# Optimization experiments

Measured on AMD Instinct MI355X. Metric: run time of the kernel, lower is better.

Reference implementation:

```python
import jax, jax.numpy as jnp
import numpy as np

N = 4096
K = 8


def setup_inputs() -> dict:
    key = jax.random.key(0)
    kA, kb, ka, kZ, kC = jax.random.split(key, 5)
    A = (jax.random.uniform(kA, (N, N)) < 0.01).astype(jnp.float32)
    beta = jax.random.normal(kb, (N,), dtype=jnp.float32)
    a = jax.random.normal(ka, (1,), dtype=jnp.float32)
    Z = jax.random.normal(kZ, (K, N), dtype=jnp.float32)
    C = jax.random.normal(kC, (N, K), dtype=jnp.float32)
    return {"A": A, "beta": beta, "a": a, "Z": Z, "C": C}


def reference(A, beta, a, Z, C):
    # beta_ij = beta_i + beta_j  -> [N, N]
    beta2 = beta[:, None] + beta[None, :]
    Zs = jax.nn.softmax(Z, axis=0)          # [K, N], softmax over archetypes
    Cs = jax.nn.softmax(C, axis=0)          # [N, K], softmax over nodes
    # M = (Zs @ Cs @ Zs).T -> [N, K] latent positions
    M = (Zs @ (Cs @ Zs)).T
    # Pairwise euclidean distance with the original's +1e-6 shift inside the square.
    diff = M[:, None, :] - M[None, :, :] + 1e-6   # [N, N, K]
    z_dist = jnp.sqrt(jnp.sum(diff * diff, axis=-1))  # [N, N]
    theta = beta2 - a[0] * z_dist
    sp = jax.nn.softplus(theta)
    # Zero the diagonal (theta - diag(diagonal(theta)) zeroes diag entries).
    d = jnp.arange(N)
    theta_off = theta.at[d, d].set(0.0)
    sp_off = sp.at[d, d].set(0.0)
    LL = jnp.sum(theta_off * A) - jnp.sum(sp_off)
    return LL
```

## Files before the change

### kernel.cpp

```cpp
#include <hip/hip_runtime.h>

#define N 4096
#define K 8
#define RB 64
#define CB 256
#define RCH 16
#define NCH (RB / RCH)
#define NPB 16

__device__ __forceinline__ float fast_exp2(float x) { return __builtin_amdgcn_exp2f(x); }
__device__ __forceinline__ float fast_log2(float x) { return __builtin_amdgcn_logf(x); }
__device__ __forceinline__ float fast_sqrt(float x) { return __builtin_amdgcn_sqrtf(x); }

__device__ __forceinline__ void load_lds_16B(const float* g, float* l) {
    __builtin_amdgcn_global_load_lds((const __attribute__((address_space(1))) void*)g,
                                     (__attribute__((address_space(3))) void*)l,
                                     16, 0, 0);
}

__global__ __launch_bounds__(256) void prep_stats(
    const float* __restrict__ Z, const float* __restrict__ C,
    const float* __restrict__ A, const float* __restrict__ beta,
    const float* __restrict__ a_ptr,
    float* __restrict__ ZsT, float* __restrict__ Upart, float* __restrict__ out)
{
    const int t = threadIdx.x;
    const int n = blockIdx.x * 256 + t;
    const float L2E = 1.44269504f;
    const float LN2 = 0.69314718f;

    __shared__ float zsL[256 * K];
    __shared__ float eL[256 * K];
    __shared__ float red[4][64];
    __shared__ float dsum[4];

    const float av_diag = A[(size_t)n * N + n];
    const float bn = beta[n];
    const float a_v = a_ptr[0];

    float z[K];
#pragma unroll
    for (int k = 0; k < K; ++k) z[k] = Z[k * N + n];
    float zmax = z[0];
#pragma unroll
    for (int k = 1; k < K; ++k) zmax = fmaxf(zmax, z[k]);
    float zs[K];
    float zsum = 0.f;
#pragma unroll
    for (int k = 0; k < K; ++k) { zs[k] = fast_exp2((z[k] - zmax) * L2E); zsum += zs[k]; }
    const float inv = 1.f / zsum;
#pragma unroll
    for (int k = 0; k < K; ++k) zs[k] *= inv;

    float4* zst_p = (float4*)(ZsT + (size_t)n * K);
    zst_p[0] = make_float4(zs[0], zs[1], zs[2], zs[3]);
    zst_p[1] = make_float4(zs[4], zs[5], zs[6], zs[7]);

    const float4* c_p = (const float4*)(C + (size_t)n * K);
    const float4 c0 = c_p[0], c1 = c_p[1];
    float e[K];
    e[0] = fast_exp2(c0.x * L2E); e[1] = fast_exp2(c0.y * L2E);
    e[2] = fast_exp2(c0.z * L2E); e[3] = fast_exp2(c0.w * L2E);
    e[4] = fast_exp2(c1.x * L2E); e[5] = fast_exp2(c1.y * L2E);
    e[6] = fast_exp2(c1.z * L2E); e[7] = fast_exp2(c1.w * L2E);

#pragma unroll
    for (int k = 0; k < K; ++k) { zsL[t * K + k] = zs[k]; eL[t * K + k] = e[k]; }
    __syncthreads();

    const int cell = t & 63, q = t >> 6;
    const int a = cell >> 3, b = cell & 7;
    float s = 0.f;
    const int n0 = q * 64;
#pragma unroll 4
    for (int nn = 0; nn < 64; ++nn)
        s = fmaf(zsL[(n0 + nn) * K + a], eL[(n0 + nn) * K + b], s);
    red[q][cell] = s;
    __syncthreads();
    if (t < 64)
        Upart[blockIdx.x * 64 + t] = red[0][t] + red[1][t] + red[2][t] + red[3][t];

    const float theta = fmaf(-a_v, 2.8284271247e-6f, 2.f * bn);
    const float ex = fast_exp2(theta * L2E);
    const float sp = LN2 * fast_log2(1.f + ex);
    float d = fmaf(theta, av_diag, -sp);
    for (int off = 32; off > 0; off >>= 1) d += __shfl_down(d, off, 64);
    const int lane = t & 63, wd = t >> 6;
    if (lane == 0) dsum[wd] = d;
    __syncthreads();
    if (t == 0) atomicAdd(out, -(dsum[0] + dsum[1] + dsum[2] + dsum[3]));
}

__global__ __launch_bounds__(256) void pair_ll(
    const float* __restrict__ A, const float* __restrict__ beta,
    const float* __restrict__ a_ptr, const float* __restrict__ ZsT,
    const float* __restrict__ Upart, float* __restrict__ out)
{
    const int t = threadIdx.x;
    const int lane = t & 63, w = t >> 6;
    const int i0 = blockIdx.x * RB;
    const int jbase = blockIdx.y * CB;
    const int j = jbase + t;
    const float L2E = 1.44269504f;
    const float LN2 = 0.69314718f;

    __shared__ __align__(16) float Abuf[2][RCH][CB];
    __shared__ __align__(16) float4 ntwoMi[RB][2];
    __shared__ __align__(8)  float2 rc[RB];
    __shared__ float UL[64];
    __shared__ float wsum[4];

    {
        const float* g = A + (size_t)(i0 + w * 4) * N + jbase + lane * 4;
#pragma unroll
        for (int rr = 0; rr < 4; ++rr)
            load_lds_16B(g + (size_t)rr * N, &Abuf[0][w * 4 + rr][0]);
    }

    if (t < 64) {
        float s = 0.f;
#pragma unroll
        for (int blk = 0; blk < NPB; ++blk) s += Upart[blk * 64 + t];
        UL[t] = s;
    }
    __syncthreads();

    float sinv[8];
#pragma unroll
    for (int b = 0; b < 8; ++b) {
        float s = 0.f;
#pragma unroll
        for (int a = 0; a < 8; ++a) s += UL[a * 8 + b];
        sinv[b] = 1.f / s;
    }

    const float4* zp = (const float4*)(ZsT + (size_t)j * K);
    const float4 z0 = zp[0], z1 = zp[1];
    float wv[K] = { z0.x * sinv[0], z0.y * sinv[1], z0.z * sinv[2], z0.w * sinv[3],
                    z1.x * sinv[4], z1.y * sinv[5], z1.z * sinv[6], z1.w * sinv[7] };
    float mj[K];
#pragma unroll
    for (int k = 0; k < K; ++k) {
        float acc = 0.f;
#pragma unroll
        for (int kk = 0; kk < K; ++kk) acc = fmaf(UL[k * K + kk], wv[kk], acc);
        mj[k] = acc;
    }
    float mj2 = mj[0] * mj[0];
#pragma unroll
    for (int k = 1; k < K; ++k) mj2 = fmaf(mj[k], mj[k], mj2);
    const float bjL2E = beta[j] * L2E;
    const float naL2E = -a_ptr[0] * L2E;

    if (t < RB) {
        const float4* zp2 = (const float4*)(ZsT + (size_t)(i0 + t) * K);
        const float4 y0 = zp2[0], y1 = zp2[1];
        float wr[K] = { y0.x * sinv[0], y0.y * sinv[1], y0.z * sinv[2], y0.w * sinv[3],
                        y1.x * sinv[4], y1.y * sinv[5], y1.z * sinv[6], y1.w * sinv[7] };
        float v[K];
#pragma unroll
        for (int k = 0; k < K; ++k) {
            float acc = 0.f;
#pragma unroll
            for (int kk = 0; kk < K; ++kk) acc = fmaf(UL[k * K + kk], wr[kk], acc);
            v[k] = acc + 1e-6f;
        }
        float s2 = 0.f;
#pragma unroll
        for (int k = 0; k < K; ++k) s2 = fmaf(v[k], v[k], s2);
        ntwoMi[t][0] = make_float4(-2.f * v[0], -2.f * v[1], -2.f * v[2], -2.f * v[3]);
        ntwoMi[t][1] = make_float4(-2.f * v[4], -2.f * v[5], -2.f * v[6], -2.f * v[7]);
        rc[t] = make_float2(s2, beta[i0 + t] * L2E);
    }
    __syncthreads();

    float acc_t = 0.f, acc_l = 0.f;
    int buf = 0;
    for (int c = 0; c < NCH; ++c) {
        if (c + 1 < NCH) {
            const float* g = A + (size_t)(i0 + (c + 1) * RCH + w * 4) * N + jbase + lane * 4;
#pragma unroll
            for (int rr = 0; rr < 4; ++rr)
                load_lds_16B(g + (size_t)rr * N, &Abuf[buf ^ 1][w * 4 + rr][0]);
        }
#pragma unroll
        for (int r = 0; r < RCH; ++r) {
            const int ir = c * RCH + r;
            const float av = Abuf[buf][r][t];
            const float4 tm0 = ntwoMi[ir][0];
            const float4 tm1 = ntwoMi[ir][1];
            const float2 cc = rc[ir];
            float ss = cc.x + mj2;
            ss = fmaf(tm0.x, mj[0], ss); ss = fmaf(tm0.y, mj[1], ss);
            ss = fmaf(tm0.z, mj[2], ss); ss = fmaf(tm0.w, mj[3], ss);
            ss = fmaf(tm1.x, mj[4], ss); ss = fmaf(tm1.y, mj[5], ss);
            ss = fmaf(tm1.z, mj[6], ss); ss = fmaf(tm1.w, mj[7], ss);
            ss = fmaxf(ss, 0.f);
            const float dist = fast_sqrt(ss);
            const float t2 = fmaf(naL2E, dist, cc.y + bjL2E);
            const float ex = fast_exp2(t2);
            const float lp = fast_log2(1.f + ex);
            acc_t = fmaf(t2, av, acc_t);
            acc_l += lp;
        }
        if (c + 1 < NCH) __syncthreads();
        buf ^= 1;
    }
    float acc = LN2 * (acc_t - acc_l);

    for (int off = 32; off > 0; off >>= 1) acc += __shfl_down(acc, off, 64);
    if (lane == 0) wsum[w] = acc;
    __syncthreads();
    if (t == 0) atomicAdd(out, wsum[0] + wsum[1] + wsum[2] + wsum[3]);
}

extern "C" void kernel_launch(void* const* d_in, const int* in_sizes, int n_in,
                              void* d_out, int out_size, void* d_ws, size_t ws_size,
                              hipStream_t stream)
{
    const float* A    = (const float*)d_in[0];
    const float* beta = (const float*)d_in[1];
    const float* a    = (const float*)d_in[2];
    const float* Z    = (const float*)d_in[3];
    const float* C    = (const float*)d_in[4];
    float* out = (float*)d_out;

    float* ws    = (float*)d_ws;
    float* ZsT   = ws;
    float* Upart = ws + (size_t)N * K;

    hipMemsetAsync(out, 0, sizeof(float), stream);
    prep_stats<<<NPB, 256, 0, stream>>>(Z, C, A, beta, a, ZsT, Upart, out);

    dim3 grid(N / RB, N / CB);
    pair_ll<<<grid, 256, 0, stream>>>(A, beta, a, ZsT, Upart, out);
}
```

Baseline: 115.7 us.

## Exploit pair symmetry: compute only upper-triangular tiles with transposed A

Result: slower. 121.5 us (+5.1%).

```diff
diff --git a/kernel.cpp b/kernel.cpp
--- a/kernel.cpp
+++ b/kernel.cpp
@@ -2,10 +2,11 @@
 
 #define N 4096
 #define K 8
-#define RB 64
-#define CB 256
+#define TB 128
+#define NT (N / TB)
 #define RCH 16
-#define NCH (RB / RCH)
+#define NCH (TB / RCH)
+#define TP 129
 #define NPB 16
 
 __device__ __forceinline__ float fast_exp2(float x) { return __builtin_amdgcn_exp2f(x); }
@@ -20,23 +21,15 @@
 
 __global__ __launch_bounds__(256) void prep_stats(
     const float* __restrict__ Z, const float* __restrict__ C,
-    const float* __restrict__ A, const float* __restrict__ beta,
-    const float* __restrict__ a_ptr,
-    float* __restrict__ ZsT, float* __restrict__ Upart, float* __restrict__ out)
+    float* __restrict__ ZsT, float* __restrict__ Upart)
 {
     const int t = threadIdx.x;
     const int n = blockIdx.x * 256 + t;
     const float L2E = 1.44269504f;
-    const float LN2 = 0.69314718f;
 
     __shared__ float zsL[256 * K];
     __shared__ float eL[256 * K];
     __shared__ float red[4][64];
-    __shared__ float dsum[4];
-
-    const float av_diag = A[(size_t)n * N + n];
-    const float bn = beta[n];
-    const float a_v = a_ptr[0];
 
     float z[K];
 #pragma unroll
@@ -79,16 +72,6 @@
     __syncthreads();
     if (t < 64)
         Upart[blockIdx.x * 64 + t] = red[0][t] + red[1][t] + red[2][t] + red[3][t];
-
-    const float theta = fmaf(-a_v, 2.8284271247e-6f, 2.f * bn);
-    const float ex = fast_exp2(theta * L2E);
-    const float sp = LN2 * fast_log2(1.f + ex);
-    float d = fmaf(theta, av_diag, -sp);
-    for (int off = 32; off > 0; off >>= 1) d += __shfl_down(d, off, 64);
-    const int lane = t & 63, wd = t >> 6;
-    if (lane == 0) dsum[wd] = d;
-    __syncthreads();
-    if (t == 0) atomicAdd(out, -(dsum[0] + dsum[1] + dsum[2] + dsum[3]));
 }
 
 __global__ __launch_bounds__(256) void pair_ll(
@@ -96,26 +79,85 @@
     const float* __restrict__ a_ptr, const float* __restrict__ ZsT,
     const float* __restrict__ Upart, float* __restrict__ out)
 {
+    const int ti = blockIdx.x, tj = blockIdx.y;
+    if (ti > tj) return;
+    const bool dTile = (ti == tj);
+
     const int t = threadIdx.x;
     const int lane = t & 63, w = t >> 6;
-    const int i0 = blockIdx.x * RB;
-    const int jbase = blockIdx.y * CB;
-    const int j = jbase + t;
+    const int i0 = ti * TB, jb = tj * TB;
+    const int jl = t & 127, h = t >> 7;
+    const int j = jb + jl;
     const float L2E = 1.44269504f;
     const float LN2 = 0.69314718f;
 
-    __shared__ __align__(16) float Abuf[2][RCH][CB];
-    __shared__ __align__(16) float4 ntwoMi[RB][2];
-    __shared__ __align__(8)  float2 rc[RB];
+    __shared__ __align__(16) float Abuf[2][RCH][TB];
+    __shared__ float Tbuf[2][RCH][TP];
+    __shared__ __align__(16) float4 ntwoMi[TB][2];
+    __shared__ __align__(8)  float2 rc[TB];
     __shared__ float UL[64];
     __shared__ float wsum[4];
 
-    {
-        const float* g = A + (size_t)(i0 + w * 4) * N + jbase + lane * 4;
-#pragma unroll
-        for (int rr = 0; rr < 4; ++rr)
-            load_lds_16B(g + (size_t)rr * N, &Abuf[0][w * 4 + rr][0]);
-    }
+#define STAGE_ABUF(B, CH)                                                          \
+    {                                                                              \
+        const float* g_ = A + (size_t)(i0 + (CH) * RCH + w * 4 + (lane >> 5)) * N  \
+                          + jb + (lane & 31) * 4;                                  \
+        load_lds_16B(g_,         &Abuf[B][w * 4][0]);                              \
+        load_lds_16B(g_ + 2 * N, &Abuf[B][w * 4 + 2][0]);                          \
+    }
+
+#define STAGE_TREG(CH)                                                             \
+    {                                                                              \
+        const float* g_ = A + (size_t)(jb + (t >> 1)) * N + i0 + (CH) * RCH        \
+                          + (t & 1) * 8;                                           \
+        tr0 = *(const float4*)(g_);                                                \
+        tr1 = *(const float4*)(g_ + 4);                                            \
+    }
+
+#define TBUF_WRITE(B)                                                              \
+    {                                                                              \
+        const int rb_ = (t & 1) * 8, m_ = t >> 1;                                  \
+        Tbuf[B][rb_ + 0][m_] = tr0.x; Tbuf[B][rb_ + 1][m_] = tr0.y;                \
+        Tbuf[B][rb_ + 2][m_] = tr0.z; Tbuf[B][rb_ + 3][m_] = tr0.w;                \
+        Tbuf[B][rb_ + 4][m_] = tr1.x; Tbuf[B][rb_ + 5][m_] = tr1.y;                \
+        Tbuf[B][rb_ + 6][m_] = tr1.z; Tbuf[B][rb_ + 7][m_] = tr1.w;                \
+    }
+
+#define CHUNK_COMPUTE(DIAGM)                                                       \
+    _Pragma("unroll")                                                              \
+    for (int k = 0; k < 8; ++k) {                                                  \
+        const int rl = h * 8 + k;                                                  \
+        const int il = c * RCH + rl;                                               \
+        const float av = Abuf[buf][rl][jl];                                        \
+        const float tv = Tbuf[buf][rl][jl];                                        \
+        const float4 tm0 = ntwoMi[il][0];                                          \
+        const float4 tm1 = ntwoMi[il][1];                                          \
+        const float2 cc = rc[il];                                                  \
+        float ss = cc.x + mjn2;                                                    \
+        ss = fmaf(tm0.x, mj[0], ss); ss = fmaf(tm0.y, mj[1], ss);                  \
+        ss = fmaf(tm0.z, mj[2], ss); ss = fmaf(tm0.w, mj[3], ss);                  \
+        ss = fmaf(tm1.x, mj[4], ss); ss = fmaf(tm1.y, mj[5], ss);                  \
+        ss = fmaf(tm1.z, mj[6], ss); ss = fmaf(tm1.w, mj[7], ss);                  \
+        ss = fmaxf(ss, 0.f);                                                       \
+        const float dist = fast_sqrt(ss);                                          \
+        const float t2 = fmaf(naL2E, dist, cc.y + bjL2E);                          \
+        const float ex = fast_exp2(t2);                                            \
+        const float lp = fast_log2(1.f + ex);                                      \
+        const float wgt = av + tv;                                                 \
+        if (DIAGM) {                                                               \
+            const float msk = (il < jl) ? 1.f : 0.f;                               \
+            acc_t = fmaf(t2, wgt * msk, acc_t);                                    \
+            acc_l = fmaf(msk, lp, acc_l);                                          \
+        } else {                                                                   \
+            acc_t = fmaf(t2, wgt, acc_t);                                          \
+            acc_l += lp;                                                           \
+        }                                                                          \
+    }
+
+    float4 tr0, tr1;
+
+    STAGE_ABUF(0, 0);
+    STAGE_TREG(0);
 
     if (t < 64) {
         float s = 0.f;
@@ -146,13 +188,13 @@
         for (int kk = 0; kk < K; ++kk) acc = fmaf(UL[k * K + kk], wv[kk], acc);
         mj[k] = acc;
     }
-    float mj2 = mj[0] * mj[0];
-#pragma unroll
-    for (int k = 1; k < K; ++k) mj2 = fmaf(mj[k], mj[k], mj2);
+    float mjn2 = mj[0] * mj[0];
+#pragma unroll
+    for (int k = 1; k < K; ++k) mjn2 = fmaf(mj[k], mj[k], mjn2);
     const float bjL2E = beta[j] * L2E;
     const float naL2E = -a_ptr[0] * L2E;
 
-    if (t < RB) {
+    if (t < TB) {
         const float4* zp2 = (const float4*)(ZsT + (size_t)(i0 + t) * K);
         const float4 y0 = zp2[0], y1 = zp2[1];
         float wr[K] = { y0.x * sinv[0], y0.y * sinv[1], y0.z * sinv[2], y0.w * sinv[3],
@@ -172,41 +214,22 @@
         ntwoMi[t][1] = make_float4(-2.f * v[4], -2.f * v[5], -2.f * v[6], -2.f * v[7]);
         rc[t] = make_float2(s2, beta[i0 + t] * L2E);
     }
+
+    TBUF_WRITE(0);
     __syncthreads();
 
     float acc_t = 0.f, acc_l = 0.f;
     int buf = 0;
     for (int c = 0; c < NCH; ++c) {
+        if (c + 1 < NCH) { STAGE_ABUF(buf ^ 1, c + 1); STAGE_TREG(c + 1); }
+        if (dTile) { CHUNK_COMPUTE(true) } else { CHUNK_COMPUTE(false) }
         if (c + 1 < NCH) {
-            const float* g = A + (size_t)(i0 + (c + 1) * RCH + w * 4) * N + jbase + lane * 4;
-#pragma unroll
-            for (int rr = 0; rr < 4; ++rr)
-                load_lds_16B(g + (size_t)rr * N, &Abuf[buf ^ 1][w * 4 + rr][0]);
+            TBUF_WRITE(buf ^ 1);
+            __syncthreads();
         }
-#pragma unroll
-        for (int r = 0; r < RCH; ++r) {
-            const int ir = c * RCH + r;
-            const float av = Abuf[buf][r][t];
-            const float4 tm0 = ntwoMi[ir][0];
-            const float4 tm1 = ntwoMi[ir][1];
-            const float2 cc = rc[ir];
-            float ss = cc.x + mj2;
-            ss = fmaf(tm0.x, mj[0], ss); ss = fmaf(tm0.y, mj[1], ss);
-            ss = fmaf(tm0.z, mj[2], ss); ss = fmaf(tm0.w, mj[3], ss);
-            ss = fmaf(tm1.x, mj[4], ss); ss = fmaf(tm1.y, mj[5], ss);
-            ss = fmaf(tm1.z, mj[6], ss); ss = fmaf(tm1.w, mj[7], ss);
-            ss = fmaxf(ss, 0.f);
-            const float dist = fast_sqrt(ss);
-            const float t2 = fmaf(naL2E, dist, cc.y + bjL2E);
-            const float ex = fast_exp2(t2);
-            const float lp = fast_log2(1.f + ex);
-            acc_t = fmaf(t2, av, acc_t);
-            acc_l += lp;
-        }
-        if (c + 1 < NCH) __syncthreads();
         buf ^= 1;
     }
-    float acc = LN2 * (acc_t - acc_l);
+    float acc = LN2 * (acc_t - 2.f * acc_l);
 
     for (int off = 32; off > 0; off >>= 1) acc += __shfl_down(acc, off, 64);
     if (lane == 0) wsum[w] = acc;
@@ -230,8 +253,9 @@
     float* Upart = ws + (size_t)N * K;
 
     hipMemsetAsync(out, 0, sizeof(float), stream);
-    prep_stats<<<NPB, 256, 0, stream>>>(Z, C, A, beta, a, ZsT, Upart, out);
-
-    dim3 grid(N / RB, N / CB);
+
+    prep_stats<<<NPB, 256, 0, stream>>>(Z, C, ZsT, Upart);
+
+    dim3 grid(NT, NT);
     pair_ll<<<grid, 256, 0, stream>>>(A, beta, a, ZsT, Upart, out);
 }
```
